# Kernel tuning notes

Hardware: AMD Instinct MI355X
Metric: run time of the kernel (lower is better)

## Reference

```python
import jax, jax.numpy as jnp
import numpy as np

DIM = 1024
NUM_HEADS = 16
HEAD_DIM = DIM // NUM_HEADS
SCALE = HEAD_DIM ** -0.5
EPS = 1e-5


def layernorm(x, gamma, beta):
    mu = jnp.mean(x, axis=-1, keepdims=True)
    var = jnp.mean(jnp.square(x - mu), axis=-1, keepdims=True)
    return (x - mu) * jax.lax.rsqrt(var + EPS) * gamma + beta


def setup_inputs() -> dict:
    key = jax.random.key(0)
    ks = jax.random.split(key, 12)
    B, Lq, Lk = 2, 2048, 2048
    s = 0.02
    return {
        "q": jax.random.normal(ks[0], (B, Lq, DIM), jnp.float32),
        "k": jax.random.normal(ks[1], (B, Lk, DIM), jnp.float32),
        "v": jax.random.normal(ks[2], (B, Lk, DIM), jnp.float32),
        "Wq": jax.random.normal(ks[3], (DIM, DIM), jnp.float32) * s,
        "Wk": jax.random.normal(ks[4], (DIM, DIM), jnp.float32) * s,
        "Wv": jax.random.normal(ks[5], (DIM, DIM), jnp.float32) * s,
        "gq": jnp.ones((HEAD_DIM,), jnp.float32),
        "bq": jnp.zeros((HEAD_DIM,), jnp.float32),
        "gk": jnp.ones((HEAD_DIM,), jnp.float32),
        "bk": jnp.zeros((HEAD_DIM,), jnp.float32),
        "Wo": jax.random.normal(ks[6], (DIM, DIM), jnp.float32) * s,
        "bo": jnp.zeros((DIM,), jnp.float32),
    }


def reference(q, k, v, Wq, Wk, Wv, gq, bq, gk, bk, Wo, bo):
    B, Lq, _ = q.shape
    Lk = k.shape[1]
    # projections: Linear(dim_in, dim) with no bias -> x @ W.T (W stored [out, in])
    qh = (q @ Wq.T).reshape(B, Lq, NUM_HEADS, HEAD_DIM).transpose(0, 2, 1, 3)
    kh = (k @ Wk.T).reshape(B, Lk, NUM_HEADS, HEAD_DIM).transpose(0, 2, 1, 3)
    vh = (v @ Wv.T).reshape(B, Lk, NUM_HEADS, HEAD_DIM).transpose(0, 2, 1, 3)
    # per-head LayerNorm on head_dim (QK-norm)
    qh = layernorm(qh, gq, bq) * SCALE
    kh = layernorm(kh, gk, bk)
    # sigmoid attention (no softmax, no row normalization)
    attn = jax.nn.sigmoid(jnp.einsum("bhqd,bhkd->bhqk", qh, kh))
    x = jnp.einsum("bhqk,bhkd->bhqd", attn, vh)
    x = x.transpose(0, 2, 1, 3).reshape(B, Lq, DIM)
    return x @ Wo.T + bo
```

## Files before the change

### kernel.cpp

```cpp
#include <hip/hip_runtime.h>
#include <stdint.h>

#define BATCH 2
#define SEQ   2048
#define DIM   1024
#define NH    16
#define MTOT  (BATCH*SEQ)
#define LN_EPS 1e-5f
#define Q_FOLD_SCALE (-0.1803368801111204f)

typedef __bf16 bf16x8 __attribute__((ext_vector_type(8)));
typedef float  f32x4  __attribute__((ext_vector_type(4)));

__device__ __forceinline__ unsigned short f2bf(float f) {
  uint32_t u = __float_as_uint(f);
  u += 0x7fffu + ((u >> 16) & 1u);
  return (unsigned short)(u >> 16);
}
__device__ __forceinline__ unsigned short f2bf_rh(float f) {
  uint32_t u = __float_as_uint(f) + 0x8000u;
  return (unsigned short)(u >> 16);
}

__device__ __forceinline__ void gload_lds16(const void* g, void* lds) {
  __builtin_amdgcn_global_load_lds(
      (const __attribute__((address_space(1))) uint32_t*)g,
      (__attribute__((address_space(3))) uint32_t*)lds, 16, 0, 0);
}

#define VMCNT(n) asm volatile("s_waitcnt vmcnt(" #n ")" ::: "memory")
#define BAR() do { __builtin_amdgcn_s_barrier(); __builtin_amdgcn_sched_barrier(0); } while (0)
#define DSFENCE() do {                                        \
    __builtin_amdgcn_sched_barrier(0);                        \
    asm volatile("s_waitcnt lgkmcnt(0)" ::: "memory");        \
    __builtin_amdgcn_sched_barrier(0);                        \
  } while (0)
#define ROT3(a, b, c) do { unsigned short* _tmp = (a); (a) = (b); (b) = (c); (c) = _tmp; } while (0)

__global__ void cvt_f32_bf16(const float* __restrict__ s0, unsigned short* __restrict__ d0,
                             const float* __restrict__ s1, unsigned short* __restrict__ d1,
                             const float* __restrict__ s2, unsigned short* __restrict__ d2,
                             const float* __restrict__ s3, unsigned short* __restrict__ d3,
                             int n) {
  int z = blockIdx.y;
  const float* s = z == 0 ? s0 : z == 1 ? s1 : z == 2 ? s2 : s3;
  unsigned short* d = z == 0 ? d0 : z == 1 ? d1 : z == 2 ? d2 : d3;
  if (s == nullptr) return;
  int i = (blockIdx.x * 256 + threadIdx.x) * 4;
  if (i >= n) return;
  float4 v = *(const float4*)(s + i);
  ushort4 o;
  o.x = f2bf(v.x); o.y = f2bf(v.y); o.z = f2bf(v.z); o.w = f2bf(v.w);
  *(ushort4*)(d + i) = o;
}

__global__ __launch_bounds__(256, 3)
void gemm_qkv(const unsigned short* __restrict__ Aq, const unsigned short* __restrict__ Ak,
              const unsigned short* __restrict__ Av,
              const unsigned short* __restrict__ Wqp, const unsigned short* __restrict__ Wkp,
              const unsigned short* __restrict__ Wvp,
              const float* __restrict__ gq, const float* __restrict__ bq,
              const float* __restrict__ gk, const float* __restrict__ bk,
              unsigned short* __restrict__ qh, unsigned short* __restrict__ kh,
              unsigned short* __restrict__ vT) {
  __shared__ unsigned short Asm[3][4096];
  __shared__ unsigned short Bsm[3][4096];
  const int z = blockIdx.z;
  const unsigned short* A = z == 0 ? Aq : z == 1 ? Ak : Av;
  const unsigned short* W = z == 0 ? Wqp : z == 1 ? Wkp : Wvp;
  const int t = threadIdx.x, w = t >> 6, l = t & 63, l15 = l & 15, lhi = l >> 4;
  const int wm = w >> 1, wn = w & 1;
  const int m0 = blockIdx.x * 128, n0 = blockIdx.y * 128;
  const int sr0 = t >> 2, sc = (t & 3) ^ (((t >> 2) >> 1) & 3);
  const int fsw = (l15 >> 1) & 3;

  unsigned short *ac = &Asm[0][0], *an = &Asm[1][0], *af_ = &Asm[2][0];
  unsigned short *bc = &Bsm[0][0], *bn = &Bsm[1][0], *bf_ = &Bsm[2][0];

  f32x4 acc[4][4] = {};

#define STAGE_G(ap, bp, kt) do {                                                  \
    int k0 = (kt) * 32;                                                           \
    gload_lds16(A + (size_t)(m0 + sr0) * 1024 + k0 + sc * 8, (ap) + t * 8);       \
    gload_lds16(A + (size_t)(m0 + 64 + sr0) * 1024 + k0 + sc * 8,                 \
                (ap) + (t + 256) * 8);                                            \
    gload_lds16(W + (size_t)(n0 + sr0) * 1024 + k0 + sc * 8, (bp) + t * 8);       \
    gload_lds16(W + (size_t)(n0 + 64 + sr0) * 1024 + k0 + sc * 8,                 \
                (bp) + (t + 256) * 8);                                            \
  } while (0)

  STAGE_G(ac, bc, 0);
  STAGE_G(an, bn, 1);
  for (int kt = 0; kt < 32; ++kt) {
    if (kt < 30)       { STAGE_G(af_, bf_, kt + 2); VMCNT(8); }
    else if (kt == 30) { VMCNT(4); }
    else               { VMCNT(0); }
    BAR();
    bf16x8 afr[4], bfr[4];
#pragma unroll
    for (int mi = 0; mi < 4; ++mi)
      afr[mi] = *(const bf16x8*)&ac[(wm * 64 + mi * 16 + l15) * 32 + ((lhi ^ fsw) * 8)];
#pragma unroll
    for (int ni = 0; ni < 4; ++ni)
      bfr[ni] = *(const bf16x8*)&bc[(wn * 64 + ni * 16 + l15) * 32 + ((lhi ^ fsw) * 8)];
    __builtin_amdgcn_s_setprio(1);
#pragma unroll
    for (int mi = 0; mi < 4; ++mi)
#pragma unroll
      for (int ni = 0; ni < 4; ++ni)
        acc[mi][ni] = __builtin_amdgcn_mfma_f32_16x16x32_bf16(afr[mi], bfr[ni], acc[mi][ni], 0, 0, 0);
    __builtin_amdgcn_s_setprio(0);
    BAR();
    ROT3(ac, an, af_);
    ROT3(bc, bn, bf_);
  }
#undef STAGE_G

  const int h = (n0 >> 6) + wn;
  if (z == 2) {
#pragma unroll
    for (int mi = 0; mi < 4; ++mi)
#pragma unroll
      for (int r = 0; r < 4; ++r) {
        int gm = m0 + wm * 64 + mi * 16 + lhi * 4 + r;
        int b = gm >> 11, pos = gm & 2047;
#pragma unroll
        for (int ni = 0; ni < 4; ++ni)
          vT[(((size_t)(b * NH + h)) * 64 + ni * 16 + l15) * SEQ + pos] = f2bf(acc[mi][ni][r]);
      }
  } else {
    const float* G  = z ? gk : gq;
    const float* Bt = z ? bk : bq;
    unsigned short* outp = z ? kh : qh;
    const float scl = z ? 1.f : Q_FOLD_SCALE;
    float g[4], bt[4];
#pragma unroll
    for (int ni = 0; ni < 4; ++ni) { g[ni] = G[ni * 16 + l15]; bt[ni] = Bt[ni * 16 + l15]; }
#pragma unroll
    for (int mi = 0; mi < 4; ++mi)
#pragma unroll
      for (int r = 0; r < 4; ++r) {
        float x[4], s = 0.f, s2 = 0.f;
#pragma unroll
        for (int ni = 0; ni < 4; ++ni) { x[ni] = acc[mi][ni][r]; s += x[ni]; s2 += x[ni] * x[ni]; }
#pragma unroll
        for (int msk = 1; msk < 16; msk <<= 1) {
          s  += __shfl_xor(s,  msk, 64);
          s2 += __shfl_xor(s2, msk, 64);
        }
        float mu = s * (1.f / 64.f);
        float var = s2 * (1.f / 64.f) - mu * mu;
        float rstd = rsqrtf(var + LN_EPS);
        int gm = m0 + wm * 64 + mi * 16 + lhi * 4 + r;
        int b = gm >> 11, pos = gm & 2047;
        size_t base = (((size_t)(b * NH + h)) * SEQ + pos) * 64;
#pragma unroll
        for (int ni = 0; ni < 4; ++ni) {
          float y = ((x[ni] - mu) * rstd * g[ni] + bt[ni]) * scl;
          outp[base + ni * 16 + l15] = f2bf(y);
        }
      }
  }
}

__global__ __launch_bounds__(256, 3)
void gemm_out(const unsigned short* __restrict__ A, const unsigned short* __restrict__ W,
              const float* __restrict__ bias, float* __restrict__ outf) {
  __shared__ unsigned short Asm[3][4096];
  __shared__ unsigned short Bsm[3][4096];
  const int t = threadIdx.x, w = t >> 6, l = t & 63, l15 = l & 15, lhi = l >> 4;
  const int wm = w >> 1, wn = w & 1;
  const int m0 = blockIdx.x * 128, n0 = blockIdx.y * 128;
  const int sr0 = t >> 2, sc = (t & 3) ^ (((t >> 2) >> 1) & 3);
  const int fsw = (l15 >> 1) & 3;

  unsigned short *ac = &Asm[0][0], *an = &Asm[1][0], *af_ = &Asm[2][0];
  unsigned short *bc = &Bsm[0][0], *bn = &Bsm[1][0], *bf_ = &Bsm[2][0];
  f32x4 acc[4][4] = {};

#define STAGE_G(ap, bp, kt) do {                                                  \
    int k0 = (kt) * 32;                                                           \
    gload_lds16(A + (size_t)(m0 + sr0) * 1024 + k0 + sc * 8, (ap) + t * 8);       \
    gload_lds16(A + (size_t)(m0 + 64 + sr0) * 1024 + k0 + sc * 8,                 \
                (ap) + (t + 256) * 8);                                            \
    gload_lds16(W + (size_t)(n0 + sr0) * 1024 + k0 + sc * 8, (bp) + t * 8);       \
    gload_lds16(W + (size_t)(n0 + 64 + sr0) * 1024 + k0 + sc * 8,                 \
                (bp) + (t + 256) * 8);                                            \
  } while (0)

  STAGE_G(ac, bc, 0);
  STAGE_G(an, bn, 1);
  for (int kt = 0; kt < 32; ++kt) {
    if (kt < 30)       { STAGE_G(af_, bf_, kt + 2); VMCNT(8); }
    else if (kt == 30) { VMCNT(4); }
    else               { VMCNT(0); }
    BAR();
    bf16x8 afr[4], bfr[4];
#pragma unroll
    for (int mi = 0; mi < 4; ++mi)
      afr[mi] = *(const bf16x8*)&ac[(wm * 64 + mi * 16 + l15) * 32 + ((lhi ^ fsw) * 8)];
#pragma unroll
    for (int ni = 0; ni < 4; ++ni)
      bfr[ni] = *(const bf16x8*)&bc[(wn * 64 + ni * 16 + l15) * 32 + ((lhi ^ fsw) * 8)];
    __builtin_amdgcn_s_setprio(1);
#pragma unroll
    for (int mi = 0; mi < 4; ++mi)
#pragma unroll
      for (int ni = 0; ni < 4; ++ni)
        acc[mi][ni] = __builtin_amdgcn_mfma_f32_16x16x32_bf16(afr[mi], bfr[ni], acc[mi][ni], 0, 0, 0);
    __builtin_amdgcn_s_setprio(0);
    BAR();
    ROT3(ac, an, af_);
    ROT3(bc, bn, bf_);
  }
#undef STAGE_G
  float bb[4];
#pragma unroll
  for (int ni = 0; ni < 4; ++ni) bb[ni] = bias[n0 + wn * 64 + ni * 16 + l15];
#pragma unroll
  for (int mi = 0; mi < 4; ++mi)
#pragma unroll
    for (int r = 0; r < 4; ++r) {
      int gm = m0 + wm * 64 + mi * 16 + lhi * 4 + r;
      float* op = outf + (size_t)gm * 1024 + n0 + wn * 64 + l15;
#pragma unroll
      for (int ni = 0; ni < 4; ++ni) op[ni * 16] = acc[mi][ni][r] + bb[ni];
    }
}

__global__ __launch_bounds__(512, 4)
void attn_kernel(const unsigned short* __restrict__ qh,
                 const unsigned short* __restrict__ kh,
                 const unsigned short* __restrict__ vT,
                 unsigned short* __restrict__ x) {
  __shared__ unsigned short Klds[3][4096];
  __shared__ unsigned short Vlds[3][4096];
  __shared__ unsigned short Plds[8 * 16 * 72];
  const int t = threadIdx.x, w = t >> 6, l = t & 63, l15 = l & 15, lhi = l >> 4;
  const int L = blockIdx.x;
  const int xcd = L & 7, j = L >> 3;
  const int bh = xcd * 4 + (j >> 4);
  const int qt = j & 15;
  const int b = bh >> 4;
  const unsigned short* Q = qh + (size_t)bh * SEQ * 64;
  const unsigned short* K = kh + (size_t)bh * SEQ * 64;
  const unsigned short* V = vT + (size_t)bh * 64 * SEQ;
  unsigned short* Pw = &Plds[w * 16 * 72];
  const int qbase = qt * 128 + w * 16;

  bf16x8 qf[2];
#pragma unroll
  for (int kb = 0; kb < 2; ++kb)
    qf[kb] = *(const bf16x8*)&Q[(size_t)(qbase + l15) * 64 + kb * 32 + lhi * 8];

  f32x4 o[4] = {};
  const int r0 = t >> 3, c0 = t & 7;

  unsigned short *kc = &Klds[0][0], *kn = &Klds[1][0], *kfu = &Klds[2][0];
  unsigned short *vc = &Vlds[0][0], *vn = &Vlds[1][0], *vfu = &Vlds[2][0];

#define STAGE_KV(kp, vp, kv0) do {                                                  \
    gload_lds16(K + (size_t)((kv0) + r0) * 64 + (c0 ^ (r0 & 7)) * 8, (kp) + t * 8); \
    gload_lds16(V + (size_t)r0 * SEQ + (kv0) + (c0 ^ (r0 & 7)) * 8, (vp) + t * 8);  \
  } while (0)

  STAGE_KV(kc, vc, 0);
  STAGE_KV(kn, vn, 64);
  for (int kv = 0; kv < 32; ++kv) {
    if (kv < 30)       { STAGE_KV(kfu, vfu, (kv + 2) * 64); VMCNT(4); }
    else if (kv == 30) { VMCNT(2); }
    else               { VMCNT(0); }
    BAR();

    f32x4 s[4] = {};
    __builtin_amdgcn_s_setprio(1);
#pragma unroll
    for (int ni = 0; ni < 4; ++ni)
#pragma unroll
      for (int kb = 0; kb < 2; ++kb) {
        bf16x8 kf = *(const bf16x8*)&kc[(ni * 16 + l15) * 64 + (((kb * 4 + lhi) ^ (l15 & 7)) * 8)];
        s[ni] = __builtin_amdgcn_mfma_f32_16x16x32_bf16(qf[kb], kf, s[ni], 0, 0, 0);
      }
    __builtin_amdgcn_s_setprio(0);

#pragma unroll
    for (int ni = 0; ni < 4; ++ni)
#pragma unroll
      for (int r = 0; r < 4; ++r) {
        float p = __builtin_amdgcn_rcpf(1.0f + __builtin_amdgcn_exp2f(s[ni][r]));
        Pw[(lhi * 4 + r) * 72 + ni * 16 + l15] = f2bf_rh(p);
      }
    DSFENCE();

    __builtin_amdgcn_s_setprio(1);
#pragma unroll
    for (int kq = 0; kq < 2; ++kq) {
      bf16x8 pf = *(const bf16x8*)&Pw[l15 * 72 + kq * 32 + lhi * 8];
#pragma unroll
      for (int di = 0; di < 4; ++di) {
        bf16x8 vf = *(const bf16x8*)&vc[(di * 16 + l15) * 64 + (((kq * 4 + lhi) ^ (l15 & 7)) * 8)];
        o[di] = __builtin_amdgcn_mfma_f32_16x16x32_bf16(pf, vf, o[di], 0, 0, 0);
      }
    }
    __builtin_amdgcn_s_setprio(0);
    BAR();

    ROT3(kc, kn, kfu);
    ROT3(vc, vn, vfu);
  }
#undef STAGE_KV

#pragma unroll
  for (int r = 0; r < 4; ++r) {
    int pos = qbase + lhi * 4 + r;
    size_t base = ((size_t)b * SEQ + pos) * DIM + (bh & 15) * 64;
#pragma unroll
    for (int di = 0; di < 4; ++di)
      x[base + di * 16 + l15] = f2bf(o[di][r]);
  }
}

extern "C" void kernel_launch(void* const* d_in, const int* in_sizes, int n_in,
                              void* d_out, int out_size, void* d_ws, size_t ws_size,
                              hipStream_t stream) {
  (void)in_sizes; (void)n_in; (void)out_size; (void)ws_size;
  const float* q  = (const float*)d_in[0];
  const float* k  = (const float*)d_in[1];
  const float* v  = (const float*)d_in[2];
  const float* Wq = (const float*)d_in[3];
  const float* Wk = (const float*)d_in[4];
  const float* Wv = (const float*)d_in[5];
  const float* gq = (const float*)d_in[6];
  const float* bq = (const float*)d_in[7];
  const float* gk = (const float*)d_in[8];
  const float* bk = (const float*)d_in[9];
  const float* Wo = (const float*)d_in[10];
  const float* bo = (const float*)d_in[11];
  float* out = (float*)d_out;

  char* ws = (char*)d_ws;
  const size_t MB = 1ull << 20;
  unsigned short* qb  = (unsigned short*)(ws + 0);
  unsigned short* kb  = (unsigned short*)(ws + 8  * MB);
  unsigned short* vb  = (unsigned short*)(ws + 16 * MB);
  unsigned short* Wqb = (unsigned short*)(ws + 24 * MB);
  unsigned short* Wkb = (unsigned short*)(ws + 26 * MB);
  unsigned short* Wvb = (unsigned short*)(ws + 28 * MB);
  unsigned short* Wob = (unsigned short*)(ws + 30 * MB);
  unsigned short* qhb = (unsigned short*)(ws + 32 * MB);
  unsigned short* khb = (unsigned short*)(ws + 40 * MB);
  unsigned short* vTb = (unsigned short*)(ws + 48 * MB);
  unsigned short* xb  = qb;

  const int nIn = MTOT * DIM;
  const int nW  = DIM * DIM;

  cvt_f32_bf16<<<dim3(nIn / 1024, 3), 256, 0, stream>>>(q, qb, k, kb, v, vb, nullptr, nullptr, nIn);
  cvt_f32_bf16<<<dim3(nW / 1024, 4), 256, 0, stream>>>(Wq, Wqb, Wk, Wkb, Wv, Wvb, Wo, Wob, nW);

  gemm_qkv<<<dim3(MTOT / 128, DIM / 128, 3), 256, 0, stream>>>(qb, kb, vb, Wqb, Wkb, Wvb,
                                                               gq, bq, gk, bk, qhb, khb, vTb);

  attn_kernel<<<dim3(512), 512, 0, stream>>>(qhb, khb, vTb, xb);

  gemm_out<<<dim3(MTOT / 128, DIM / 128), 256, 0, stream>>>(xb, Wob, bo, out);
}
```

Before: 133.6 us.

## Software-pipeline attention loop: overlap next QK^T with current sigmoid and PV

```diff
diff --git a/kernel.cpp b/kernel.cpp
--- a/kernel.cpp
+++ b/kernel.cpp
@@ -35,7 +35,8 @@
     asm volatile("s_waitcnt lgkmcnt(0)" ::: "memory");        \
     __builtin_amdgcn_sched_barrier(0);                        \
   } while (0)
-#define ROT3(a, b, c) do { unsigned short* _tmp = (a); (a) = (b); (b) = (c); (c) = _tmp; } while (0)
+#define ROT3(a, b, c) do { unsigned short* _t3 = (a); (a) = (b); (b) = (c); (c) = _t3; } while (0)
+#define ROT4(a, b, c, d) do { unsigned short* _t4 = (a); (a) = (b); (b) = (c); (c) = (d); (d) = _t4; } while (0)
 
 __global__ void cvt_f32_bf16(const float* __restrict__ s0, unsigned short* __restrict__ d0,
                              const float* __restrict__ s1, unsigned short* __restrict__ d1,
@@ -234,7 +235,7 @@
                  const unsigned short* __restrict__ vT,
                  unsigned short* __restrict__ x) {
   __shared__ unsigned short Klds[3][4096];
-  __shared__ unsigned short Vlds[3][4096];
+  __shared__ unsigned short Vlds[4][4096];
   __shared__ unsigned short Plds[8 * 16 * 72];
   const int t = threadIdx.x, w = t >> 6, l = t & 63, l15 = l & 15, lhi = l >> 4;
   const int L = blockIdx.x;
@@ -254,60 +255,108 @@
     qf[kb] = *(const bf16x8*)&Q[(size_t)(qbase + l15) * 64 + kb * 32 + lhi * 8];
 
   f32x4 o[4] = {};
+  f32x4 sA[4], sB[4];
   const int r0 = t >> 3, c0 = t & 7;
 
-  unsigned short *kc = &Klds[0][0], *kn = &Klds[1][0], *kfu = &Klds[2][0];
-  unsigned short *vc = &Vlds[0][0], *vn = &Vlds[1][0], *vfu = &Vlds[2][0];
-
-#define STAGE_KV(kp, vp, kv0) do {                                                  \
-    gload_lds16(K + (size_t)((kv0) + r0) * 64 + (c0 ^ (r0 & 7)) * 8, (kp) + t * 8); \
-    gload_lds16(V + (size_t)r0 * SEQ + (kv0) + (c0 ^ (r0 & 7)) * 8, (vp) + t * 8);  \
+  unsigned short *kc = &Klds[0][0], *kn = &Klds[1][0], *kf_ = &Klds[2][0];
+  unsigned short *vp = &Vlds[3][0], *vc = &Vlds[0][0], *vn = &Vlds[1][0], *vf_ = &Vlds[2][0];
+
+#define STAGE_KV(kp, vpp, kv0) do {                                                  \
+    gload_lds16(K + (size_t)((kv0) + r0) * 64 + (c0 ^ (r0 & 7)) * 8, (kp) + t * 8);  \
+    gload_lds16(V + (size_t)r0 * SEQ + (kv0) + (c0 ^ (r0 & 7)) * 8, (vpp) + t * 8);  \
+  } while (0)
+
+#define QKT(DST) do {                                                                \
+    __builtin_amdgcn_s_setprio(1);                                                   \
+    _Pragma("unroll")                                                                \
+    for (int ni = 0; ni < 4; ++ni) {                                                 \
+      DST[ni] = (f32x4){};                                                           \
+      _Pragma("unroll")                                                              \
+      for (int kb = 0; kb < 2; ++kb) {                                               \
+        bf16x8 kfr = *(const bf16x8*)&kc[(ni * 16 + l15) * 64 + (((kb * 4 + lhi) ^ (l15 & 7)) * 8)]; \
+        DST[ni] = __builtin_amdgcn_mfma_f32_16x16x32_bf16(qf[kb], kfr, DST[ni], 0, 0, 0); \
+      }                                                                              \
+    }                                                                                \
+    __builtin_amdgcn_s_setprio(0);                                                   \
+  } while (0)
+
+#define SIG(SRC) do {                                                                \
+    _Pragma("unroll")                                                                \
+    for (int ni = 0; ni < 4; ++ni)                                                   \
+      _Pragma("unroll")                                                              \
+      for (int r = 0; r < 4; ++r) {                                                  \
+        float p = __builtin_amdgcn_rcpf(1.0f + __builtin_amdgcn_exp2f(SRC[ni][r]));  \
+        Pw[(lhi * 4 + r) * 72 + ni * 16 + l15] = f2bf_rh(p);                         \
+      }                                                                              \
+  } while (0)
+
+#define PV(vptr) do {                                                                \
+    __builtin_amdgcn_s_setprio(1);                                                   \
+    _Pragma("unroll")                                                                \
+    for (int kq = 0; kq < 2; ++kq) {                                                 \
+      bf16x8 pf = *(const bf16x8*)&Pw[l15 * 72 + kq * 32 + lhi * 8];                 \
+      _Pragma("unroll")                                                              \
+      for (int di = 0; di < 4; ++di) {                                               \
+        bf16x8 vfr = *(const bf16x8*)&(vptr)[(di * 16 + l15) * 64 + (((kq * 4 + lhi) ^ (l15 & 7)) * 8)]; \
+        o[di] = __builtin_amdgcn_mfma_f32_16x16x32_bf16(pf, vfr, o[di], 0, 0, 0);    \
+      }                                                                              \
+    }                                                                                \
+    __builtin_amdgcn_s_setprio(0);                                                   \
+  } while (0)
+
+#define STEP_FULL(SN, SC, TV) do {                                                   \
+    STAGE_KV(kf_, vf_, ((TV) + 2) * 64);                                             \
+    VMCNT(4);                                                                        \
+    BAR();                                                                           \
+    QKT(SN);                                                                         \
+    SIG(SC);                                                                         \
+    DSFENCE();                                                                       \
+    PV(vp);                                                                          \
+    BAR();                                                                           \
+    ROT3(kc, kn, kf_);                                                               \
+    ROT4(vp, vc, vn, vf_);                                                           \
   } while (0)
 
   STAGE_KV(kc, vc, 0);
   STAGE_KV(kn, vn, 64);
-  for (int kv = 0; kv < 32; ++kv) {
-    if (kv < 30)       { STAGE_KV(kfu, vfu, (kv + 2) * 64); VMCNT(4); }
-    else if (kv == 30) { VMCNT(2); }
-    else               { VMCNT(0); }
-    BAR();
-
-    f32x4 s[4] = {};
-    __builtin_amdgcn_s_setprio(1);
-#pragma unroll
-    for (int ni = 0; ni < 4; ++ni)
-#pragma unroll
-      for (int kb = 0; kb < 2; ++kb) {
-        bf16x8 kf = *(const bf16x8*)&kc[(ni * 16 + l15) * 64 + (((kb * 4 + lhi) ^ (l15 & 7)) * 8)];
-        s[ni] = __builtin_amdgcn_mfma_f32_16x16x32_bf16(qf[kb], kf, s[ni], 0, 0, 0);
-      }
-    __builtin_amdgcn_s_setprio(0);
-
-#pragma unroll
-    for (int ni = 0; ni < 4; ++ni)
-#pragma unroll
-      for (int r = 0; r < 4; ++r) {
-        float p = __builtin_amdgcn_rcpf(1.0f + __builtin_amdgcn_exp2f(s[ni][r]));
-        Pw[(lhi * 4 + r) * 72 + ni * 16 + l15] = f2bf_rh(p);
-      }
-    DSFENCE();
-
-    __builtin_amdgcn_s_setprio(1);
-#pragma unroll
-    for (int kq = 0; kq < 2; ++kq) {
-      bf16x8 pf = *(const bf16x8*)&Pw[l15 * 72 + kq * 32 + lhi * 8];
-#pragma unroll
-      for (int di = 0; di < 4; ++di) {
-        bf16x8 vf = *(const bf16x8*)&vc[(di * 16 + l15) * 64 + (((kq * 4 + lhi) ^ (l15 & 7)) * 8)];
-        o[di] = __builtin_amdgcn_mfma_f32_16x16x32_bf16(pf, vf, o[di], 0, 0, 0);
-      }
-    }
-    __builtin_amdgcn_s_setprio(0);
-    BAR();
-
-    ROT3(kc, kn, kfu);
-    ROT3(vc, vn, vfu);
+  STAGE_KV(kf_, vf_, 128);
+  VMCNT(4);
+  BAR();
+  QKT(sA);
+  BAR();
+  ROT3(kc, kn, kf_);
+  ROT4(vp, vc, vn, vf_);
+
+  for (int tt = 0; tt < 14; ++tt) {
+    const int t1 = 2 * tt + 1;
+    STEP_FULL(sB, sA, t1);
+    STEP_FULL(sA, sB, t1 + 1);
   }
+  STEP_FULL(sB, sA, 29);
+  VMCNT(2);
+  BAR();
+  QKT(sA);
+  SIG(sB);
+  DSFENCE();
+  PV(vp);
+  BAR();
+  ROT3(kc, kn, kf_);
+  ROT4(vp, vc, vn, vf_);
+  VMCNT(0);
+  BAR();
+  QKT(sB);
+  SIG(sA);
+  DSFENCE();
+  PV(vp);
+  DSFENCE();
+  SIG(sB);
+  DSFENCE();
+  PV(vc);
+
+#undef STEP_FULL
+#undef PV
+#undef SIG
+#undef QKT
 #undef STAGE_KV
 
 #pragma unroll
```

Result: no change. 133.7 us (+0.1%).
